# Kernel tuning notes

Hardware: AMD Instinct MI355X
Metric: run time of the kernel (lower is better)

Reference implementation:

```python
import jax, jax.numpy as jnp
import numpy as np

S, H = 8192, 2048


def setup_inputs() -> dict:
    key = jax.random.key(0)
    k1, k2, k3, k4, k5 = jax.random.split(key, 5)
    encoder_outputs = jax.random.normal(k1, (S, 1, H), dtype=jnp.float32)
    hidden = jax.random.normal(k2, (H,), dtype=jnp.float32)
    # nn.Linear(2H, H): weight [H, 2H], bias [H]
    lim = 1.0 / np.sqrt(2 * H)
    W_att = jax.random.uniform(k3, (H, 2 * H), dtype=jnp.float32, minval=-lim, maxval=lim)
    b_att = jax.random.uniform(k4, (H,), dtype=jnp.float32, minval=-lim, maxval=lim)
    w = jax.random.normal(k5, (1, H), dtype=jnp.float32)
    return {"encoder_outputs": encoder_outputs, "hidden": hidden,
            "W_att": W_att, "b_att": b_att, "w": w}


def reference(encoder_outputs, hidden, W_att, b_att, w):
    # Original loops over source_len: score_i = w . (Linear(cat(hidden, enc_i)))
    # Vectorized: build [S, 2H] once, one GEMM, one dot, one softmax.
    enc = encoder_outputs[:, 0, :]                      # [S, H]
    h = jnp.broadcast_to(hidden[None, :], enc.shape)    # [S, H]
    x = jnp.concatenate([h, enc], axis=1)               # [S, 2H]
    res = x @ W_att.T + b_att                           # [S, H]
    scores = res @ w[0]                                 # [S]
    attn = jax.nn.softmax(scores, axis=0)               # softmax over source_len
    return attn[None, None, :]                          # [1, 1, S]
```

## Files before the change

kernel.cpp:

```cpp
#include <hip/hip_runtime.h>
#include <math.h>

#define SS 8192
#define HH 2048


__global__ void zero_v2(float* __restrict__ v2) {
    int i = blockIdx.x * blockDim.x + threadIdx.x;
    if (i < HH) v2[i] = 0.0f;
}

__global__ void colsum_kernel(const float* __restrict__ W,
                              const float* __restrict__ w,
                              float* __restrict__ v2) {
    const int col  = blockIdx.x * 256 + threadIdx.x;
    const int row0 = blockIdx.y * 64;
    const float* base = W + (size_t)row0 * (2 * HH) + HH + col;
    float acc = 0.0f;
#pragma unroll 8
    for (int j = 0; j < 64; ++j) {
        acc += w[row0 + j] * base[(size_t)j * (2 * HH)];
    }
    atomicAdd(&v2[col], acc);
}

__global__ void rowdot_kernel(const float* __restrict__ enc,
                              const float* __restrict__ v2,
                              float* __restrict__ scores) {
    const int wave = threadIdx.x >> 6;
    const int lane = threadIdx.x & 63;
    const int row  = blockIdx.x * 4 + wave;
    const float4* e = (const float4*)(enc + (size_t)row * HH);
    const float4* v = (const float4*)v2;
    float acc = 0.0f;
#pragma unroll
    for (int i = 0; i < 8; ++i) {
        float4 a = e[lane + i * 64];
        float4 b = v[lane + i * 64];
        acc += a.x * b.x + a.y * b.y + a.z * b.z + a.w * b.w;
    }
    for (int off = 32; off > 0; off >>= 1)
        acc += __shfl_down(acc, off);
    if (lane == 0) scores[row] = acc;
}

__global__ void softmax_kernel(float* __restrict__ buf) {
    __shared__ float red[16];
    const int tid  = threadIdx.x;
    const int lane = tid & 63;
    const int wid  = tid >> 6;

    float vals[8];
    float m = -INFINITY;
#pragma unroll
    for (int i = 0; i < 8; ++i) {
        vals[i] = buf[tid + i * 1024];
        m = fmaxf(m, vals[i]);
    }
    for (int off = 1; off < 64; off <<= 1)
        m = fmaxf(m, __shfl_xor(m, off));
    if (lane == 0) red[wid] = m;
    __syncthreads();
    if (tid == 0) {
        float mm = red[0];
        for (int i = 1; i < 16; ++i) mm = fmaxf(mm, red[i]);
        red[0] = mm;
    }
    __syncthreads();
    m = red[0];

    float s = 0.0f;
#pragma unroll
    for (int i = 0; i < 8; ++i) {
        vals[i] = __expf(vals[i] - m);
        s += vals[i];
    }
    for (int off = 1; off < 64; off <<= 1)
        s += __shfl_xor(s, off);
    __syncthreads();
    if (lane == 0) red[wid] = s;
    __syncthreads();
    if (tid == 0) {
        float ss = 0.0f;
        for (int i = 0; i < 16; ++i) ss += red[i];
        red[0] = ss;
    }
    __syncthreads();
    const float inv = 1.0f / red[0];
#pragma unroll
    for (int i = 0; i < 8; ++i)
        buf[tid + i * 1024] = vals[i] * inv;
}

extern "C" void kernel_launch(void* const* d_in, const int* in_sizes, int n_in,
                              void* d_out, int out_size, void* d_ws, size_t ws_size,
                              hipStream_t stream) {
    const float* enc   = (const float*)d_in[0];
    const float* W_att = (const float*)d_in[2];
    const float* w     = (const float*)d_in[4];

    float* out = (float*)d_out;
    float* v2  = (float*)d_ws;

    hipLaunchKernelGGL(zero_v2,        dim3(8),      dim3(256),  0, stream, v2);
    hipLaunchKernelGGL(colsum_kernel,  dim3(8, 32),  dim3(256),  0, stream, W_att, w, v2);
    hipLaunchKernelGGL(rowdot_kernel,  dim3(2048),   dim3(256),  0, stream, enc, v2, out);
    hipLaunchKernelGGL(softmax_kernel, dim3(1),      dim3(1024), 0, stream, out);
}
```

Before: 120.4 us.

## Fuse attention-score pipeline into one cooperative kernel with grid syncs

```diff
diff --git a/kernel.cpp b/kernel.cpp
--- a/kernel.cpp
+++ b/kernel.cpp
@@ -1,95 +1,108 @@
 #include <hip/hip_runtime.h>
+#include <hip/hip_cooperative_groups.h>
 #include <math.h>
+
+namespace cg = cooperative_groups;
 
 #define SS 8192
 #define HH 2048
 
 
-__global__ void zero_v2(float* __restrict__ v2) {
-    int i = blockIdx.x * blockDim.x + threadIdx.x;
-    if (i < HH) v2[i] = 0.0f;
-}
+__global__ void __launch_bounds__(256, 1) fused_attn(
+    const float* __restrict__ enc,
+    const float* __restrict__ W,
+    const float* __restrict__ w,
+    float* __restrict__ out,
+    float* __restrict__ ws)
+{
+    cg::grid_group grid = cg::this_grid();
+    const int tid  = threadIdx.x;
+    const int bid  = blockIdx.x;
+    const int gtid = bid * 256 + tid;
 
-__global__ void colsum_kernel(const float* __restrict__ W,
-                              const float* __restrict__ w,
-                              float* __restrict__ v2) {
-    const int col  = blockIdx.x * 256 + threadIdx.x;
-    const int row0 = blockIdx.y * 64;
-    const float* base = W + (size_t)row0 * (2 * HH) + HH + col;
-    float acc = 0.0f;
+    float* v2     = ws;
+    float* scores = ws + HH;
+
+    if (gtid < HH) v2[gtid] = 0.0f;
+    grid.sync();
+
+    {
+        const int bx   = bid & 7;
+        const int by   = bid >> 3;
+        const int col  = bx * 256 + tid;
+        const int row0 = by * 64;
+        const float* base = W + (size_t)row0 * (2 * HH) + HH + col;
+        float acc = 0.0f;
 #pragma unroll 8
-    for (int j = 0; j < 64; ++j) {
-        acc += w[row0 + j] * base[(size_t)j * (2 * HH)];
+        for (int j = 0; j < 64; ++j)
+            acc += w[row0 + j] * base[(size_t)j * (2 * HH)];
+        atomicAdd(&v2[col], acc);
     }
-    atomicAdd(&v2[col], acc);
-}
+    grid.sync();
 
-__global__ void rowdot_kernel(const float* __restrict__ enc,
-                              const float* __restrict__ v2,
-                              float* __restrict__ scores) {
-    const int wave = threadIdx.x >> 6;
-    const int lane = threadIdx.x & 63;
-    const int row  = blockIdx.x * 4 + wave;
-    const float4* e = (const float4*)(enc + (size_t)row * HH);
-    const float4* v = (const float4*)v2;
-    float acc = 0.0f;
+    {
+        const int wave = gtid >> 6;
+        const int lane = tid & 63;
+        const float4* v = (const float4*)v2;
+        float4 vb[8];
 #pragma unroll
-    for (int i = 0; i < 8; ++i) {
-        float4 a = e[lane + i * 64];
-        float4 b = v[lane + i * 64];
-        acc += a.x * b.x + a.y * b.y + a.z * b.z + a.w * b.w;
+        for (int i = 0; i < 8; ++i) vb[i] = v[lane + i * 64];
+
+        for (int rr = 0; rr < 8; ++rr) {
+            const int row = wave * 8 + rr;
+            const float4* e = (const float4*)(enc + (size_t)row * HH);
+            float acc = 0.0f;
+#pragma unroll
+            for (int i = 0; i < 8; ++i) {
+                float4 a = e[lane + i * 64];
+                acc += a.x * vb[i].x + a.y * vb[i].y + a.z * vb[i].z + a.w * vb[i].w;
+            }
+#pragma unroll
+            for (int off = 32; off > 0; off >>= 1)
+                acc += __shfl_down(acc, off);
+            if (lane == 0) scores[row] = acc;
+        }
     }
-    for (int off = 32; off > 0; off >>= 1)
-        acc += __shfl_down(acc, off);
-    if (lane == 0) scores[row] = acc;
-}
+    grid.sync();
 
-__global__ void softmax_kernel(float* __restrict__ buf) {
-    __shared__ float red[16];
-    const int tid  = threadIdx.x;
-    const int lane = tid & 63;
-    const int wid  = tid >> 6;
+    if (bid == 0) {
+        __shared__ float red[4];
+        const int lane = tid & 63;
+        const int wid  = tid >> 6;
 
-    float vals[8];
-    float m = -INFINITY;
+        float vals[32];
+        float m = -INFINITY;
 #pragma unroll
-    for (int i = 0; i < 8; ++i) {
-        vals[i] = buf[tid + i * 1024];
-        m = fmaxf(m, vals[i]);
+        for (int i = 0; i < 32; ++i) {
+            vals[i] = scores[tid + i * 256];
+            m = fmaxf(m, vals[i]);
+        }
+#pragma unroll
+        for (int off = 1; off < 64; off <<= 1)
+            m = fmaxf(m, __shfl_xor(m, off));
+        if (lane == 0) red[wid] = m;
+        __syncthreads();
+        m = fmaxf(fmaxf(red[0], red[1]), fmaxf(red[2], red[3]));
+
+        float s = 0.0f;
+#pragma unroll
+        for (int i = 0; i < 32; ++i) {
+            vals[i] = __expf(vals[i] - m);
+            s += vals[i];
+        }
+#pragma unroll
+        for (int off = 1; off < 64; off <<= 1)
+            s += __shfl_xor(s, off);
+        __syncthreads();
+        if (lane == 0) red[wid] = s;
+        __syncthreads();
+        s = red[0] + red[1] + red[2] + red[3];
+
+        const float inv = 1.0f / s;
+#pragma unroll
+        for (int i = 0; i < 32; ++i)
+            out[tid + i * 256] = vals[i] * inv;
     }
-    for (int off = 1; off < 64; off <<= 1)
-        m = fmaxf(m, __shfl_xor(m, off));
-    if (lane == 0) red[wid] = m;
-    __syncthreads();
-    if (tid == 0) {
-        float mm = red[0];
-        for (int i = 1; i < 16; ++i) mm = fmaxf(mm, red[i]);
-        red[0] = mm;
-    }
-    __syncthreads();
-    m = red[0];
-
-    float s = 0.0f;
-#pragma unroll
-    for (int i = 0; i < 8; ++i) {
-        vals[i] = __expf(vals[i] - m);
-        s += vals[i];
-    }
-    for (int off = 1; off < 64; off <<= 1)
-        s += __shfl_xor(s, off);
-    __syncthreads();
-    if (lane == 0) red[wid] = s;
-    __syncthreads();
-    if (tid == 0) {
-        float ss = 0.0f;
-        for (int i = 0; i < 16; ++i) ss += red[i];
-        red[0] = ss;
-    }
-    __syncthreads();
-    const float inv = 1.0f / red[0];
-#pragma unroll
-    for (int i = 0; i < 8; ++i)
-        buf[tid + i * 1024] = vals[i] * inv;
 }
 
 extern "C" void kernel_launch(void* const* d_in, const int* in_sizes, int n_in,
@@ -100,10 +113,8 @@
     const float* w     = (const float*)d_in[4];
 
     float* out = (float*)d_out;
-    float* v2  = (float*)d_ws;
+    float* ws  = (float*)d_ws;
 
-    hipLaunchKernelGGL(zero_v2,        dim3(8),      dim3(256),  0, stream, v2);
-    hipLaunchKernelGGL(colsum_kernel,  dim3(8, 32),  dim3(256),  0, stream, W_att, w, v2);
-    hipLaunchKernelGGL(rowdot_kernel,  dim3(2048),   dim3(256),  0, stream, enc, v2, out);
-    hipLaunchKernelGGL(softmax_kernel, dim3(1),      dim3(1024), 0, stream, out);
+    void* args[] = { (void*)&enc, (void*)&W_att, (void*)&w, (void*)&out, (void*)&ws };
+    hipLaunchCooperativeKernel((void*)fused_attn, dim3(256), dim3(256), args, 0, stream);
 }
```

New measurement: 221.9 us. +84.2%, slower.

## Replace atomic column-sum with two-partial LDS reduction and drop zero kernel

Applied to the files above, without the earlier changes.

```diff
diff --git a/kernel.cpp b/kernel.cpp
--- a/kernel.cpp
+++ b/kernel.cpp
@@ -4,47 +4,76 @@
 #define SS 8192
 #define HH 2048
 
+__global__ void __launch_bounds__(256) colsum_kernel(
+    const float* __restrict__ W,
+    const float* __restrict__ w,
+    float* __restrict__ pp)
+{
+    const int cg = blockIdx.x & 127;
+    const int rh = blockIdx.x >> 7;
+    const int c4 = threadIdx.x & 3;
+    const int rg = threadIdx.x >> 2;
+    const int col0 = cg * 16 + c4 * 4;
+    const int row0 = rh * 1024 + rg * 16;
 
-__global__ void zero_v2(float* __restrict__ v2) {
-    int i = blockIdx.x * blockDim.x + threadIdx.x;
-    if (i < HH) v2[i] = 0.0f;
+    const float* base = W + (size_t)row0 * (2 * HH) + HH + col0;
+    float4 acc = make_float4(0.f, 0.f, 0.f, 0.f);
+#pragma unroll
+    for (int i = 0; i < 16; ++i) {
+        const float wi = w[row0 + i];
+        const float4 a = *(const float4*)(base + (size_t)i * (2 * HH));
+        acc.x += wi * a.x; acc.y += wi * a.y;
+        acc.z += wi * a.z; acc.w += wi * a.w;
+    }
+
+    __shared__ float4 lds[256];
+    lds[threadIdx.x] = acc;
+    __syncthreads();
+    for (int off = 128; off >= 4; off >>= 1) {
+        if (threadIdx.x < off) {
+            float4 o = lds[threadIdx.x + off];
+            float4 m = lds[threadIdx.x];
+            m.x += o.x; m.y += o.y; m.z += o.z; m.w += o.w;
+            lds[threadIdx.x] = m;
+        }
+        __syncthreads();
+    }
+    if (threadIdx.x < 4)
+        ((float4*)(pp + (size_t)rh * HH))[cg * 4 + threadIdx.x] = lds[threadIdx.x];
 }
 
-__global__ void colsum_kernel(const float* __restrict__ W,
-                              const float* __restrict__ w,
-                              float* __restrict__ v2) {
-    const int col  = blockIdx.x * 256 + threadIdx.x;
-    const int row0 = blockIdx.y * 64;
-    const float* base = W + (size_t)row0 * (2 * HH) + HH + col;
-    float acc = 0.0f;
-#pragma unroll 8
-    for (int j = 0; j < 64; ++j) {
-        acc += w[row0 + j] * base[(size_t)j * (2 * HH)];
-    }
-    atomicAdd(&v2[col], acc);
-}
-
-__global__ void rowdot_kernel(const float* __restrict__ enc,
-                              const float* __restrict__ v2,
-                              float* __restrict__ scores) {
+__global__ void __launch_bounds__(256) rowdot_kernel(
+    const float* __restrict__ enc,
+    const float* __restrict__ pp,
+    float* __restrict__ scores)
+{
     const int wave = threadIdx.x >> 6;
     const int lane = threadIdx.x & 63;
     const int row  = blockIdx.x * 4 + wave;
-    const float4* e = (const float4*)(enc + (size_t)row * HH);
-    const float4* v = (const float4*)v2;
+
+    const float4* p0 = (const float4*)pp;
+    const float4* p1 = (const float4*)(pp + HH);
+    const float4* e  = (const float4*)(enc + (size_t)row * HH);
+
     float acc = 0.0f;
 #pragma unroll
     for (int i = 0; i < 8; ++i) {
-        float4 a = e[lane + i * 64];
-        float4 b = v[lane + i * 64];
-        acc += a.x * b.x + a.y * b.y + a.z * b.z + a.w * b.w;
+        const float4 a  = e[lane + i * 64];
+        const float4 b0 = p0[lane + i * 64];
+        const float4 b1 = p1[lane + i * 64];
+        acc += a.x * (b0.x + b1.x) + a.y * (b0.y + b1.y)
+             + a.z * (b0.z + b1.z) + a.w * (b0.w + b1.w);
     }
+#pragma unroll
     for (int off = 32; off > 0; off >>= 1)
         acc += __shfl_down(acc, off);
     if (lane == 0) scores[row] = acc;
 }
 
-__global__ void softmax_kernel(float* __restrict__ buf) {
+__global__ void __launch_bounds__(1024) softmax_kernel(
+    const float* __restrict__ scores,
+    float* __restrict__ out)
+{
     __shared__ float red[16];
     const int tid  = threadIdx.x;
     const int lane = tid & 63;
@@ -54,20 +83,16 @@
     float m = -INFINITY;
 #pragma unroll
     for (int i = 0; i < 8; ++i) {
-        vals[i] = buf[tid + i * 1024];
+        vals[i] = scores[tid + i * 1024];
         m = fmaxf(m, vals[i]);
     }
+#pragma unroll
     for (int off = 1; off < 64; off <<= 1)
         m = fmaxf(m, __shfl_xor(m, off));
     if (lane == 0) red[wid] = m;
     __syncthreads();
-    if (tid == 0) {
-        float mm = red[0];
-        for (int i = 1; i < 16; ++i) mm = fmaxf(mm, red[i]);
-        red[0] = mm;
-    }
-    __syncthreads();
-    m = red[0];
+#pragma unroll
+    for (int i = 0; i < 16; ++i) m = fmaxf(m, red[i]);
 
     float s = 0.0f;
 #pragma unroll
@@ -75,21 +100,20 @@
         vals[i] = __expf(vals[i] - m);
         s += vals[i];
     }
+#pragma unroll
     for (int off = 1; off < 64; off <<= 1)
         s += __shfl_xor(s, off);
     __syncthreads();
     if (lane == 0) red[wid] = s;
     __syncthreads();
-    if (tid == 0) {
-        float ss = 0.0f;
-        for (int i = 0; i < 16; ++i) ss += red[i];
-        red[0] = ss;
-    }
-    __syncthreads();
-    const float inv = 1.0f / red[0];
+    float tot = 0.0f;
+#pragma unroll
+    for (int i = 0; i < 16; ++i) tot += red[i];
+
+    const float inv = 1.0f / tot;
 #pragma unroll
     for (int i = 0; i < 8; ++i)
-        buf[tid + i * 1024] = vals[i] * inv;
+        out[tid + i * 1024] = vals[i] * inv;
 }
 
 extern "C" void kernel_launch(void* const* d_in, const int* in_sizes, int n_in,
@@ -99,11 +123,12 @@
     const float* W_att = (const float*)d_in[2];
     const float* w     = (const float*)d_in[4];
 
-    float* out = (float*)d_out;
-    float* v2  = (float*)d_ws;
+    float* out    = (float*)d_out;
+    float* ws     = (float*)d_ws;
+    float* pp     = ws;
+    float* scores = ws + 2 * HH;
 
-    hipLaunchKernelGGL(zero_v2,        dim3(8),      dim3(256),  0, stream, v2);
-    hipLaunchKernelGGL(colsum_kernel,  dim3(8, 32),  dim3(256),  0, stream, W_att, w, v2);
-    hipLaunchKernelGGL(rowdot_kernel,  dim3(2048),   dim3(256),  0, stream, enc, v2, out);
-    hipLaunchKernelGGL(softmax_kernel, dim3(1),      dim3(1024), 0, stream, out);
+    hipLaunchKernelGGL(colsum_kernel,  dim3(256),  dim3(256),  0, stream, W_att, w, pp);
+    hipLaunchKernelGGL(rowdot_kernel,  dim3(2048), dim3(256),  0, stream, enc, pp, scores);
+    hipLaunchKernelGGL(softmax_kernel, dim3(1),    dim3(1024), 0, stream, scores, out);
 }
```

Result: no change. 122.1 us (+1.4%).
